# Performance work log

Measured on AMD Instinct MI355X. Metric: run time of the kernel, lower is better.

## Reference

```python
import jax, jax.numpy as jnp
import numpy as np

B, D, H, W = 1, 128, 128, 128
TIME_STEP = 7


def identity_grid(b, d, h, w):
    # torch grid_sample convention: last dim is (x, y, z) = (W, H, D), in [-1, 1]
    z = jnp.linspace(-1.0, 1.0, d, dtype=jnp.float32)
    y = jnp.linspace(-1.0, 1.0, h, dtype=jnp.float32)
    x = jnp.linspace(-1.0, 1.0, w, dtype=jnp.float32)
    zz, yy, xx = jnp.meshgrid(z, y, x, indexing='ij')
    g = jnp.stack([xx, yy, zz], axis=-1)  # [d, h, w, 3]
    return jnp.broadcast_to(g[None], (b, d, h, w, 3))


def grid_sample_3d(vol, grid):
    # vol: [B, C, D, H, W]; grid: [B, D, H, W, 3] with (x, y, z) in [-1, 1]
    # mode='bilinear' (trilinear), padding_mode='border', align_corners=True
    Bv, C, Dv, Hv, Wv = vol.shape
    x = (grid[..., 0] + 1.0) * 0.5 * (Wv - 1)
    y = (grid[..., 1] + 1.0) * 0.5 * (Hv - 1)
    z = (grid[..., 2] + 1.0) * 0.5 * (Dv - 1)
    x0f, y0f, z0f = jnp.floor(x), jnp.floor(y), jnp.floor(z)
    wx = (x - x0f)[:, None]  # [B,1,D,H,W]
    wy = (y - y0f)[:, None]
    wz = (z - z0f)[:, None]
    x0 = jnp.clip(x0f, 0, Wv - 1).astype(jnp.int32)
    x1 = jnp.clip(x0f + 1, 0, Wv - 1).astype(jnp.int32)
    y0 = jnp.clip(y0f, 0, Hv - 1).astype(jnp.int32)
    y1 = jnp.clip(y0f + 1, 0, Hv - 1).astype(jnp.int32)
    z0 = jnp.clip(z0f, 0, Dv - 1).astype(jnp.int32)
    z1 = jnp.clip(z0f + 1, 0, Dv - 1).astype(jnp.int32)

    vol_flat = vol.reshape(Bv, C, Dv * Hv * Wv)

    def gather(zi, yi, xi):
        lin = (zi * Hv + yi) * Wv + xi  # [B, D, H, W]
        lin = jnp.broadcast_to(lin.reshape(Bv, 1, -1), (Bv, C, Dv * Hv * Wv))
        return jnp.take_along_axis(vol_flat, lin, axis=2).reshape(Bv, C, Dv, Hv, Wv)

    c000 = gather(z0, y0, x0); c001 = gather(z0, y0, x1)
    c010 = gather(z0, y1, x0); c011 = gather(z0, y1, x1)
    c100 = gather(z1, y0, x0); c101 = gather(z1, y0, x1)
    c110 = gather(z1, y1, x0); c111 = gather(z1, y1, x1)

    top = (c000 * (1 - wx) + c001 * wx) * (1 - wy) + (c010 * (1 - wx) + c011 * wx) * wy
    bot = (c100 * (1 - wx) + c101 * wx) * (1 - wy) + (c110 * (1 - wx) + c111 * wx) * wy
    return top * (1 - wz) + bot * wz


def setup_inputs() -> dict:
    key = jax.random.key(0)
    velocity = jax.random.normal(key, (B, 3, D, H, W), dtype=jnp.float32)
    sample_grid = identity_grid(B, D, H, W)
    return {"velocity": velocity, "sample_grid": sample_grid}


def reference(velocity, sample_grid):
    flow = velocity / (2.0 ** TIME_STEP)
    for _ in range(TIME_STEP):
        grid = sample_grid + jnp.transpose(flow, (0, 2, 3, 4, 1))
        flow = flow + grid_sample_3d(flow, grid)
    return flow
```

## Files before the change

### kernel.cpp

```cpp
#include <hip/hip_runtime.h>


#define DD 128
#define HH 128
#define WW 128
#define NVOX (DD * HH * WW)
#define NELEM (3 * NVOX)
#define SCALE 63.5f
#define INV128 (1.0f / 128.0f)

__device__ __forceinline__ int blk_addr4(int xc, int yc, int zc) {
    return ((zc >> 1) << 15) + ((yc >> 1) << 9) + ((xc >> 1) << 3)
         + ((zc & 1) << 2) + ((yc & 1) << 1) + (xc & 1);
}

__global__ void extract_tables_kernel(const float* __restrict__ grid,
                                      float* __restrict__ tbl) {
    int i = threadIdx.x;
    if (i < 128) {
        tbl[i] = grid[3 * i + 0];
    } else if (i < 256) {
        int h = i - 128;
        tbl[128 + h] = grid[(h * WW) * 3 + 1];
    } else if (i < 384) {
        int d = i - 256;
        tbl[256 + d] = grid[(d * HH * WW) * 3 + 2];
    }
}

__global__ __launch_bounds__(256) void first_step_fused_kernel(
    const float* __restrict__ vel,
    const float* __restrict__ tbl,
    float4* __restrict__ dst4) {
    __shared__ float s_tx[128], s_ty[128], s_tz[128];
    int tid = threadIdx.x;
    if (tid < 128) {
        s_tx[tid] = tbl[tid];
        s_tz[tid] = tbl[256 + tid];
    } else {
        s_ty[tid - 128] = tbl[tid];
    }
    __syncthreads();

    int gid = blockIdx.x * blockDim.x + threadIdx.x;
    if (gid >= NVOX) return;

    int phase = gid & 7;
    int sv = gid >> 3;
    int x = ((sv & 63) << 1) | (phase & 1);
    int y = (((sv >> 6) & 63) << 1) | ((phase >> 1) & 1);
    int z = ((sv >> 12) << 1) | ((phase >> 2) & 1);
    int lin = (z * HH + y) * WW + x;

    float4 f;
    f.x = vel[lin] * INV128;
    f.y = vel[NVOX + lin] * INV128;
    f.z = vel[2 * NVOX + lin] * INV128;
    f.w = 0.0f;

    float xs = (s_tx[x] + f.x + 1.0f) * SCALE;
    float ys = (s_ty[y] + f.y + 1.0f) * SCALE;
    float zs = (s_tz[z] + f.z + 1.0f) * SCALE;

    float x0f = floorf(xs), y0f = floorf(ys), z0f = floorf(zs);
    float wx = xs - x0f, wy = ys - y0f, wz = zs - z0f;
    float omx = 1.0f - wx, omy = 1.0f - wy, omz = 1.0f - wz;

    int x0 = min(max((int)x0f, 0), WW - 1);
    int x1 = min(max((int)x0f + 1, 0), WW - 1);
    int y0 = min(max((int)y0f, 0), HH - 1);
    int y1 = min(max((int)y0f + 1, 0), HH - 1);
    int z0 = min(max((int)z0f, 0), DD - 1);
    int z1 = min(max((int)z0f + 1, 0), DD - 1);

    int o00 = (z0 * HH + y0) * WW;
    int o01 = (z0 * HH + y1) * WW;
    int o10 = (z1 * HH + y0) * WW;
    int o11 = (z1 * HH + y1) * WW;

    float vx, vy, vzv;
    #pragma unroll
    for (int c = 0; c < 3; ++c) {
        const float* p = vel + c * NVOX;
        float c000 = p[o00 + x0] * INV128, c001 = p[o00 + x1] * INV128;
        float c010 = p[o01 + x0] * INV128, c011 = p[o01 + x1] * INV128;
        float c100 = p[o10 + x0] * INV128, c101 = p[o10 + x1] * INV128;
        float c110 = p[o11 + x0] * INV128, c111 = p[o11 + x1] * INV128;
        float t = (c000 * omx + c001 * wx) * omy + (c010 * omx + c011 * wx) * wy;
        float b = (c100 * omx + c101 * wx) * omy + (c110 * omx + c111 * wx) * wy;
        float v = t * omz + b * wz;
        if (c == 0) vx = v; else if (c == 1) vy = v; else vzv = v;
    }

    float4 o;
    o.x = f.x + vx;
    o.y = f.y + vy;
    o.z = f.z + vzv;
    o.w = 0.0f;
    dst4[gid] = o;
}

template <bool PLANAR_OUT>
__global__ __launch_bounds__(256) void warp_step_blk_kernel(
    const float4* __restrict__ src,
    const float* __restrict__ tbl,
    float4* __restrict__ dst4,
    float* __restrict__ dstp) {
    __shared__ float s_tx[128], s_ty[128], s_tz[128];
    int tid = threadIdx.x;
    if (tid < 128) {
        s_tx[tid] = tbl[tid];
        s_tz[tid] = tbl[256 + tid];
    } else {
        s_ty[tid - 128] = tbl[tid];
    }
    __syncthreads();

    int gid = blockIdx.x * blockDim.x + threadIdx.x;
    if (gid >= NVOX) return;

    int phase = gid & 7;
    int sv = gid >> 3;
    int x = ((sv & 63) << 1) | (phase & 1);
    int y = (((sv >> 6) & 63) << 1) | ((phase >> 1) & 1);
    int z = ((sv >> 12) << 1) | ((phase >> 2) & 1);

    float4 f = src[gid];

    float xs = (s_tx[x] + f.x + 1.0f) * SCALE;
    float ys = (s_ty[y] + f.y + 1.0f) * SCALE;
    float zs = (s_tz[z] + f.z + 1.0f) * SCALE;

    float x0f = floorf(xs), y0f = floorf(ys), z0f = floorf(zs);
    float wx = xs - x0f, wy = ys - y0f, wz = zs - z0f;
    float omx = 1.0f - wx, omy = 1.0f - wy, omz = 1.0f - wz;

    int x0 = min(max((int)x0f, 0), WW - 1);
    int x1 = min(max((int)x0f + 1, 0), WW - 1);
    int y0 = min(max((int)y0f, 0), HH - 1);
    int y1 = min(max((int)y0f + 1, 0), HH - 1);
    int z0 = min(max((int)z0f, 0), DD - 1);
    int z1 = min(max((int)z0f + 1, 0), DD - 1);

    float4 c000 = src[blk_addr4(x0, y0, z0)];
    float4 c001 = src[blk_addr4(x1, y0, z0)];
    float4 c010 = src[blk_addr4(x0, y1, z0)];
    float4 c011 = src[blk_addr4(x1, y1, z0)];
    float4 c100 = src[blk_addr4(x0, y0, z1)];
    float4 c101 = src[blk_addr4(x1, y0, z1)];
    float4 c110 = src[blk_addr4(x0, y1, z1)];
    float4 c111 = src[blk_addr4(x1, y1, z1)];

    float vx, vy, vzv;
    {
        float t, b;
        t = (c000.x * omx + c001.x * wx) * omy + (c010.x * omx + c011.x * wx) * wy;
        b = (c100.x * omx + c101.x * wx) * omy + (c110.x * omx + c111.x * wx) * wy;
        vx = t * omz + b * wz;
        t = (c000.y * omx + c001.y * wx) * omy + (c010.y * omx + c011.y * wx) * wy;
        b = (c100.y * omx + c101.y * wx) * omy + (c110.y * omx + c111.y * wx) * wy;
        vy = t * omz + b * wz;
        t = (c000.z * omx + c001.z * wx) * omy + (c010.z * omx + c011.z * wx) * wy;
        b = (c100.z * omx + c101.z * wx) * omy + (c110.z * omx + c111.z * wx) * wy;
        vzv = t * omz + b * wz;
    }

    if (PLANAR_OUT) {
        int lin = (z * HH + y) * WW + x;
        dstp[lin] = f.x + vx;
        dstp[NVOX + lin] = f.y + vy;
        dstp[2 * NVOX + lin] = f.z + vzv;
    } else {
        float4 o;
        o.x = f.x + vx;
        o.y = f.y + vy;
        o.z = f.z + vzv;
        o.w = 0.0f;
        dst4[gid] = o;
    }
}

__global__ __launch_bounds__(256) void init_flow_aos_kernel(
    const float* __restrict__ vel, float4* __restrict__ flow) {
    int i = blockIdx.x * blockDim.x + threadIdx.x;
    if (i >= NVOX) return;
    float4 f;
    f.x = vel[i] * INV128;
    f.y = vel[NVOX + i] * INV128;
    f.z = vel[2 * NVOX + i] * INV128;
    f.w = 0.0f;
    flow[i] = f;
}

template <bool PLANAR_OUT>
__global__ __launch_bounds__(256) void warp_step_aos_kernel(
    const float4* __restrict__ src, const float* __restrict__ grid,
    float4* __restrict__ dst4, float* __restrict__ dstp) {
    int idx = blockIdx.x * blockDim.x + threadIdx.x;
    if (idx >= NVOX) return;

    float4 f = src[idx];
    float gx = grid[3 * idx + 0];
    float gy = grid[3 * idx + 1];
    float gz = grid[3 * idx + 2];

    float x = (gx + f.x + 1.0f) * SCALE;
    float y = (gy + f.y + 1.0f) * SCALE;
    float z = (gz + f.z + 1.0f) * SCALE;

    float x0f = floorf(x), y0f = floorf(y), z0f = floorf(z);
    float wx = x - x0f, wy = y - y0f, wz = z - z0f;
    float omx = 1.0f - wx, omy = 1.0f - wy, omz = 1.0f - wz;

    int x0 = min(max((int)x0f, 0), WW - 1);
    int x1 = min(max((int)x0f + 1, 0), WW - 1);
    int y0 = min(max((int)y0f, 0), HH - 1);
    int y1 = min(max((int)y0f + 1, 0), HH - 1);
    int z0 = min(max((int)z0f, 0), DD - 1);
    int z1 = min(max((int)z0f + 1, 0), DD - 1);

    const float4* r00 = src + (z0 * HH + y0) * WW;
    const float4* r01 = src + (z0 * HH + y1) * WW;
    const float4* r10 = src + (z1 * HH + y0) * WW;
    const float4* r11 = src + (z1 * HH + y1) * WW;

    float4 c000 = r00[x0], c001 = r00[x1];
    float4 c010 = r01[x0], c011 = r01[x1];
    float4 c100 = r10[x0], c101 = r10[x1];
    float4 c110 = r11[x0], c111 = r11[x1];

    float vx, vy, vzv;
    {
        float t, b;
        t = (c000.x * omx + c001.x * wx) * omy + (c010.x * omx + c011.x * wx) * wy;
        b = (c100.x * omx + c101.x * wx) * omy + (c110.x * omx + c111.x * wx) * wy;
        vx = t * omz + b * wz;
        t = (c000.y * omx + c001.y * wx) * omy + (c010.y * omx + c011.y * wx) * wy;
        b = (c100.y * omx + c101.y * wx) * omy + (c110.y * omx + c111.y * wx) * wy;
        vy = t * omz + b * wz;
        t = (c000.z * omx + c001.z * wx) * omy + (c010.z * omx + c011.z * wx) * wy;
        b = (c100.z * omx + c101.z * wx) * omy + (c110.z * omx + c111.z * wx) * wy;
        vzv = t * omz + b * wz;
    }

    if (PLANAR_OUT) {
        dstp[idx] = f.x + vx;
        dstp[NVOX + idx] = f.y + vy;
        dstp[2 * NVOX + idx] = f.z + vzv;
    } else {
        float4 o;
        o.x = f.x + vx; o.y = f.y + vy; o.z = f.z + vzv; o.w = 0.0f;
        dst4[idx] = o;
    }
}

__global__ __launch_bounds__(256) void init_flow_kernel(
    const float* __restrict__ vel, float* __restrict__ flow) {
    int i = blockIdx.x * blockDim.x + threadIdx.x;
    if (i < NELEM) flow[i] = vel[i] * INV128;
}

__global__ __launch_bounds__(256) void warp_step_kernel(
    const float* __restrict__ src, const float* __restrict__ grid,
    float* __restrict__ dst) {
    int idx = blockIdx.x * blockDim.x + threadIdx.x;
    if (idx >= NVOX) return;

    float fx = src[idx];
    float fy = src[NVOX + idx];
    float fz = src[2 * NVOX + idx];
    float gx = grid[idx * 3 + 0];
    float gy = grid[idx * 3 + 1];
    float gz = grid[idx * 3 + 2];

    float x = (gx + fx + 1.0f) * SCALE;
    float y = (gy + fy + 1.0f) * SCALE;
    float z = (gz + fz + 1.0f) * SCALE;

    float x0f = floorf(x), y0f = floorf(y), z0f = floorf(z);
    float wx = x - x0f, wy = y - y0f, wz = z - z0f;

    int x0 = min(max((int)x0f, 0), WW - 1);
    int x1 = min(max((int)x0f + 1, 0), WW - 1);
    int y0 = min(max((int)y0f, 0), HH - 1);
    int y1 = min(max((int)y0f + 1, 0), HH - 1);
    int z0 = min(max((int)z0f, 0), DD - 1);
    int z1 = min(max((int)z0f + 1, 0), DD - 1);

    int o00 = (z0 * HH + y0) * WW;
    int o01 = (z0 * HH + y1) * WW;
    int o10 = (z1 * HH + y0) * WW;
    int o11 = (z1 * HH + y1) * WW;

    float omx = 1.0f - wx, omy = 1.0f - wy, omz = 1.0f - wz;

    #pragma unroll
    for (int c = 0; c < 3; ++c) {
        const float* p = src + c * NVOX;
        float c000 = p[o00 + x0], c001 = p[o00 + x1];
        float c010 = p[o01 + x0], c011 = p[o01 + x1];
        float c100 = p[o10 + x0], c101 = p[o10 + x1];
        float c110 = p[o11 + x0], c111 = p[o11 + x1];
        float top = (c000 * omx + c001 * wx) * omy + (c010 * omx + c011 * wx) * wy;
        float bot = (c100 * omx + c101 * wx) * omy + (c110 * omx + c111 * wx) * wy;
        float val = top * omz + bot * wz;
        float fcur = (c == 0) ? fx : ((c == 1) ? fy : fz);
        dst[c * NVOX + idx] = fcur + val;
    }
}

extern "C" void kernel_launch(void* const* d_in, const int* in_sizes, int n_in,
                              void* d_out, int out_size, void* d_ws, size_t ws_size,
                              hipStream_t stream) {
    const float* vel  = (const float*)d_in[0];
    const float* grid = (const float*)d_in[1];
    float* out = (float*)d_out;

    const size_t aos_bytes = (size_t)NVOX * 16;
    const size_t tbl_bytes = 4096;

    if (ws_size >= 2 * aos_bytes + tbl_bytes) {
        float* tbl = (float*)d_ws;
        float4* A = (float4*)((char*)d_ws + tbl_bytes);
        float4* B = A + NVOX;

        extract_tables_kernel<<<1, 384, 0, stream>>>(grid, tbl);
        first_step_fused_kernel<<<(NVOX + 255) / 256, 256, 0, stream>>>(vel, tbl, A);

        const float4* cur = A;
        for (int it = 0; it < 5; ++it) {
            float4* nxt = (it & 1) ? A : B;
            warp_step_blk_kernel<false><<<(NVOX + 255) / 256, 256, 0, stream>>>(
                cur, tbl, nxt, nullptr);
            cur = nxt;
        }
        warp_step_blk_kernel<true><<<(NVOX + 255) / 256, 256, 0, stream>>>(
            cur, tbl, nullptr, out);
    } else if (ws_size >= 2 * aos_bytes) {
        float4* A = (float4*)d_ws;
        float4* B = A + NVOX;
        init_flow_aos_kernel<<<(NVOX + 255) / 256, 256, 0, stream>>>(vel, A);
        const float4* cur = A;
        for (int it = 0; it < 6; ++it) {
            float4* nxt = (it & 1) ? A : B;
            warp_step_aos_kernel<false><<<(NVOX + 255) / 256, 256, 0, stream>>>(
                cur, grid, nxt, nullptr);
            cur = nxt;
        }
        warp_step_aos_kernel<true><<<(NVOX + 255) / 256, 256, 0, stream>>>(
            cur, grid, nullptr, out);
    } else {
        float* ws = (float*)d_ws;
        init_flow_kernel<<<(NELEM + 255) / 256, 256, 0, stream>>>(vel, ws);
        const float* cur = ws;
        for (int it = 0; it < 7; ++it) {
            float* nxt = (it & 1) ? ws : out;
            warp_step_kernel<<<(NVOX + 255) / 256, 256, 0, stream>>>(cur, grid, nxt);
            cur = nxt;
        }
    }
}
```

Before: 217.9 us.

## Fuse table extraction into first step and stage velocity halo tile in LDS

After: 200.2 us. 1.09x faster.

```diff
diff --git a/kernel.cpp b/kernel.cpp
--- a/kernel.cpp
+++ b/kernel.cpp
@@ -14,53 +14,59 @@
          + ((zc & 1) << 2) + ((yc & 1) << 1) + (xc & 1);
 }
 
-__global__ void extract_tables_kernel(const float* __restrict__ grid,
-                                      float* __restrict__ tbl) {
-    int i = threadIdx.x;
-    if (i < 128) {
-        tbl[i] = grid[3 * i + 0];
-    } else if (i < 256) {
-        int h = i - 128;
-        tbl[128 + h] = grid[(h * WW) * 3 + 1];
-    } else if (i < 384) {
-        int d = i - 256;
-        tbl[256 + d] = grid[(d * HH * WW) * 3 + 2];
-    }
-}
-
-__global__ __launch_bounds__(256) void first_step_fused_kernel(
+__global__ __launch_bounds__(512) void fused_step1_kernel(
     const float* __restrict__ vel,
-    const float* __restrict__ tbl,
-    float4* __restrict__ dst4) {
-    __shared__ float s_tx[128], s_ty[128], s_tz[128];
+    const float* __restrict__ grid,
+    float4* __restrict__ dst4,
+    float* __restrict__ tbl) {
+    __shared__ float s_vel[16 * 16 * 16 * 3];
+
     int tid = threadIdx.x;
-    if (tid < 128) {
-        s_tx[tid] = tbl[tid];
-        s_tz[tid] = tbl[256 + tid];
-    } else {
-        s_ty[tid - 128] = tbl[tid];
+
+    if (blockIdx.x == 0 && tid < 128) {
+        tbl[tid]       = grid[3 * tid + 0];
+        tbl[128 + tid] = grid[(tid * WW) * 3 + 1];
+        tbl[256 + tid] = grid[(tid * HH * WW) * 3 + 2];
+    }
+
+    int btx = blockIdx.x & 15, bty = (blockIdx.x >> 4) & 15, btz = blockIdx.x >> 8;
+    int tx = btx << 3, ty = bty << 3, tz = btz << 3;
+    int ox = tx - 4, oy = ty - 4, oz = tz - 4;
+
+    #pragma unroll
+    for (int c = 0; c < 3; ++c) {
+        const float* p = vel + c * NVOX;
+        #pragma unroll
+        for (int k = 0; k < 8; ++k) {
+            int cell = tid + (k << 9);
+            int xx = cell & 15, yy = (cell >> 4) & 15, zz = cell >> 8;
+            int gx = min(max(ox + xx, 0), WW - 1);
+            int gy = min(max(oy + yy, 0), HH - 1);
+            int gz = min(max(oz + zz, 0), DD - 1);
+            s_vel[cell * 3 + c] = p[(gz * HH + gy) * WW + gx] * INV128;
+        }
     }
     __syncthreads();
 
-    int gid = blockIdx.x * blockDim.x + threadIdx.x;
-    if (gid >= NVOX) return;
-
-    int phase = gid & 7;
-    int sv = gid >> 3;
-    int x = ((sv & 63) << 1) | (phase & 1);
-    int y = (((sv >> 6) & 63) << 1) | ((phase >> 1) & 1);
-    int z = ((sv >> 12) << 1) | ((phase >> 2) & 1);
-    int lin = (z * HH + y) * WW + x;
-
-    float4 f;
-    f.x = vel[lin] * INV128;
-    f.y = vel[NVOX + lin] * INV128;
-    f.z = vel[2 * NVOX + lin] * INV128;
-    f.w = 0.0f;
-
-    float xs = (s_tx[x] + f.x + 1.0f) * SCALE;
-    float ys = (s_ty[y] + f.y + 1.0f) * SCALE;
-    float zs = (s_tz[z] + f.z + 1.0f) * SCALE;
+    int phase = tid & 7;
+    int svl = tid >> 3;
+    int vx = tx + (((svl & 3) << 1) | (phase & 1));
+    int vy = ty + ((((svl >> 2) & 3) << 1) | ((phase >> 1) & 1));
+    int vz = tz + ((((svl >> 4) & 3) << 1) | ((phase >> 2) & 1));
+
+    int ls = (((vz - oz) * 16) + (vy - oy)) * 16 + (vx - ox);
+    float fx = s_vel[ls * 3 + 0];
+    float fy = s_vel[ls * 3 + 1];
+    float fz = s_vel[ls * 3 + 2];
+
+    int lin = (vz * HH + vy) * WW + vx;
+    float gxv = grid[3 * lin + 0];
+    float gyv = grid[3 * lin + 1];
+    float gzv = grid[3 * lin + 2];
+
+    float xs = (gxv + fx + 1.0f) * SCALE;
+    float ys = (gyv + fy + 1.0f) * SCALE;
+    float zs = (gzv + fz + 1.0f) * SCALE;
 
     float x0f = floorf(xs), y0f = floorf(ys), z0f = floorf(zs);
     float wx = xs - x0f, wy = ys - y0f, wz = zs - z0f;
@@ -73,31 +79,55 @@
     int z0 = min(max((int)z0f, 0), DD - 1);
     int z1 = min(max((int)z0f + 1, 0), DD - 1);
 
-    int o00 = (z0 * HH + y0) * WW;
-    int o01 = (z0 * HH + y1) * WW;
-    int o10 = (z1 * HH + y0) * WW;
-    int o11 = (z1 * HH + y1) * WW;
-
-    float vx, vy, vzv;
-    #pragma unroll
-    for (int c = 0; c < 3; ++c) {
-        const float* p = vel + c * NVOX;
-        float c000 = p[o00 + x0] * INV128, c001 = p[o00 + x1] * INV128;
-        float c010 = p[o01 + x0] * INV128, c011 = p[o01 + x1] * INV128;
-        float c100 = p[o10 + x0] * INV128, c101 = p[o10 + x1] * INV128;
-        float c110 = p[o11 + x0] * INV128, c111 = p[o11 + x1] * INV128;
-        float t = (c000 * omx + c001 * wx) * omy + (c010 * omx + c011 * wx) * wy;
-        float b = (c100 * omx + c101 * wx) * omy + (c110 * omx + c111 * wx) * wy;
-        float v = t * omz + b * wz;
-        if (c == 0) vx = v; else if (c == 1) vy = v; else vzv = v;
+    float vxo, vyo, vzo;
+    bool in_tile = (x0 >= ox) && (x1 <= ox + 15) &&
+                   (y0 >= oy) && (y1 <= oy + 15) &&
+                   (z0 >= oz) && (z1 <= oz + 15);
+    if (in_tile) {
+        int i000 = ((z0 - oz) * 16 + (y0 - oy)) * 16 + (x0 - ox);
+        int i001 = ((z0 - oz) * 16 + (y0 - oy)) * 16 + (x1 - ox);
+        int i010 = ((z0 - oz) * 16 + (y1 - oy)) * 16 + (x0 - ox);
+        int i011 = ((z0 - oz) * 16 + (y1 - oy)) * 16 + (x1 - ox);
+        int i100 = ((z1 - oz) * 16 + (y0 - oy)) * 16 + (x0 - ox);
+        int i101 = ((z1 - oz) * 16 + (y0 - oy)) * 16 + (x1 - ox);
+        int i110 = ((z1 - oz) * 16 + (y1 - oy)) * 16 + (x0 - ox);
+        int i111 = ((z1 - oz) * 16 + (y1 - oy)) * 16 + (x1 - ox);
+        #pragma unroll
+        for (int c = 0; c < 3; ++c) {
+            float c000 = s_vel[i000 * 3 + c], c001 = s_vel[i001 * 3 + c];
+            float c010 = s_vel[i010 * 3 + c], c011 = s_vel[i011 * 3 + c];
+            float c100 = s_vel[i100 * 3 + c], c101 = s_vel[i101 * 3 + c];
+            float c110 = s_vel[i110 * 3 + c], c111 = s_vel[i111 * 3 + c];
+            float t = (c000 * omx + c001 * wx) * omy + (c010 * omx + c011 * wx) * wy;
+            float b = (c100 * omx + c101 * wx) * omy + (c110 * omx + c111 * wx) * wy;
+            float v = t * omz + b * wz;
+            if (c == 0) vxo = v; else if (c == 1) vyo = v; else vzo = v;
+        }
+    } else {
+        int o00 = (z0 * HH + y0) * WW;
+        int o01 = (z0 * HH + y1) * WW;
+        int o10 = (z1 * HH + y0) * WW;
+        int o11 = (z1 * HH + y1) * WW;
+        #pragma unroll
+        for (int c = 0; c < 3; ++c) {
+            const float* p = vel + c * NVOX;
+            float c000 = p[o00 + x0] * INV128, c001 = p[o00 + x1] * INV128;
+            float c010 = p[o01 + x0] * INV128, c011 = p[o01 + x1] * INV128;
+            float c100 = p[o10 + x0] * INV128, c101 = p[o10 + x1] * INV128;
+            float c110 = p[o11 + x0] * INV128, c111 = p[o11 + x1] * INV128;
+            float t = (c000 * omx + c001 * wx) * omy + (c010 * omx + c011 * wx) * wy;
+            float b = (c100 * omx + c101 * wx) * omy + (c110 * omx + c111 * wx) * wy;
+            float v = t * omz + b * wz;
+            if (c == 0) vxo = v; else if (c == 1) vyo = v; else vzo = v;
+        }
     }
 
     float4 o;
-    o.x = f.x + vx;
-    o.y = f.y + vy;
-    o.z = f.z + vzv;
+    o.x = fx + vxo;
+    o.y = fy + vyo;
+    o.z = fz + vzo;
     o.w = 0.0f;
-    dst4[gid] = o;
+    dst4[blk_addr4(vx, vy, vz)] = o;
 }
 
 template <bool PLANAR_OUT>
@@ -324,8 +354,7 @@
         float4* A = (float4*)((char*)d_ws + tbl_bytes);
         float4* B = A + NVOX;
 
-        extract_tables_kernel<<<1, 384, 0, stream>>>(grid, tbl);
-        first_step_fused_kernel<<<(NVOX + 255) / 256, 256, 0, stream>>>(vel, tbl, A);
+        fused_step1_kernel<<<4096, 512, 0, stream>>>(vel, grid, A, tbl);
 
         const float4* cur = A;
         for (int it = 0; it < 5; ++it) {
```
